# Kernel tuning notes

Hardware: AMD Instinct MI355X
Metric: run time of the kernel (lower is better)

Reference implementation:

```python
import jax, jax.numpy as jnp
import numpy as np
from jax import lax

B, N_ENT, D_ENT = 64, 512, 256
C_SCAT, C_MAP, W = 32, 18, 64
N_RES = 4


def conv2d(x, w, stride, pad):
    return lax.conv_general_dilated(x, w, (stride, stride), [(pad, pad), (pad, pad)],
                                    dimension_numbers=('NCHW', 'OIHW', 'NCHW'))


def batchnorm(x, g, b, eps=1e-5):
    # training-mode BN (batch statistics), matching nn.BatchNorm2d default train()
    mu = x.mean((0, 2, 3), keepdims=True)
    var = x.var((0, 2, 3), keepdims=True)
    return g[None, :, None, None] * (x - mu) * lax.rsqrt(var + eps) + b[None, :, None, None]


def setup_inputs() -> dict:
    key = jax.random.key(0)
    ks = jax.random.split(key, 24)
    s = 0.05
    inp = {
        'x': jax.random.uniform(ks[0], (B, C_MAP, W, W), jnp.float32),
        'entity_embeddings': jax.random.normal(ks[1], (B, N_ENT, D_ENT), jnp.float32),
        'entity_x_y': jax.random.randint(ks[2], (B, N_ENT, 16), 0, 2, jnp.int32),
        'conv1_w': jax.random.normal(ks[3], (C_SCAT, D_ENT), jnp.float32) * s,
        'project_w': jax.random.normal(ks[4], (32, C_SCAT + C_MAP, 1, 1), jnp.float32) * s,
        'project_b': jnp.zeros((32,), jnp.float32),
        'ds1_w': jax.random.normal(ks[5], (64, 32, 4, 4), jnp.float32) * s,
        'ds1_b': jnp.zeros((64,), jnp.float32),
        'ds2_w': jax.random.normal(ks[6], (128, 64, 4, 4), jnp.float32) * s,
        'ds2_b': jnp.zeros((128,), jnp.float32),
        'ds3_w': jax.random.normal(ks[7], (128, 128, 4, 4), jnp.float32) * s,
        'ds3_b': jnp.zeros((128,), jnp.float32),
        'res_conv1_w': jax.random.normal(ks[8], (N_RES, 128, 128, 3, 3), jnp.float32) * s,
        'res_bn1_g': jnp.ones((N_RES, 128), jnp.float32),
        'res_bn1_b': jnp.zeros((N_RES, 128), jnp.float32),
        'res_conv2_w': jax.random.normal(ks[9], (N_RES, 128, 128, 3, 3), jnp.float32) * s,
        'res_bn2_g': jnp.ones((N_RES, 128), jnp.float32),
        'res_bn2_b': jnp.zeros((N_RES, 128), jnp.float32),
        'fc_w': jax.random.normal(ks[10], (256, 8 * 8 * 128), jnp.float32) * s,
        'fc_b': jnp.zeros((256,), jnp.float32),
    }
    return inp


def _scatter(entity_embeddings, entity_x_y, conv1_w):
    # reduced = relu(Conv1d(256->32, k=1)) on entity dim
    reduced = jax.nn.relu(jnp.einsum('bnd,cd->bnc', entity_embeddings, conv1_w))  # [B,N,32]
    bits = entity_x_y
    pow2 = (2 ** jnp.arange(7, -1, -1)).astype(jnp.int32)
    xv = (bits[..., :8] * pow2).sum(-1) // 4   # [B,N] in 0..63
    yv = (bits[..., 8:] * pow2).sum(-1) // 4
    valid = (bits[..., 0] != -1000000000)
    reduced = reduced * valid[..., None].astype(reduced.dtype)
    b_idx = jnp.arange(entity_embeddings.shape[0], dtype=jnp.int32)[:, None]
    flat = (b_idx * (W * W) + yv * W + xv).reshape(-1)
    scat = jax.ops.segment_sum(reduced.reshape(-1, C_SCAT), flat, num_segments=entity_embeddings.shape[0] * W * W)
    return scat.reshape(-1, W, W, C_SCAT).transpose(0, 3, 1, 2)  # [B,32,W,W]


def reference(x, entity_embeddings, entity_x_y, conv1_w, project_w, project_b,
              ds1_w, ds1_b, ds2_w, ds2_b, ds3_w, ds3_b,
              res_conv1_w, res_bn1_g, res_bn1_b, res_conv2_w, res_bn2_g, res_bn2_b,
              fc_w, fc_b):
    scatter_map = _scatter(entity_embeddings, entity_x_y, conv1_w)
    h = jnp.concatenate([scatter_map, x], axis=1)  # [B,50,64,64]
    h = jax.nn.relu(conv2d(h, project_w, 1, 0) + project_b[None, :, None, None])
    h = jax.nn.relu(conv2d(h, ds1_w, 2, 1) + ds1_b[None, :, None, None])   # [B,64,32,32]
    h = jax.nn.relu(conv2d(h, ds2_w, 2, 1) + ds2_b[None, :, None, None])   # [B,128,16,16]
    h = jax.nn.relu(conv2d(h, ds3_w, 2, 1) + ds3_b[None, :, None, None])   # [B,128,8,8]
    map_skip = h
    for i in range(N_RES):
        identity = h
        o = batchnorm(conv2d(h, res_conv1_w[i], 1, 1), res_bn1_g[i], res_bn1_b[i])
        o = jax.nn.relu(o)
        o = batchnorm(conv2d(o, res_conv2_w[i], 1, 1), res_bn2_g[i], res_bn2_b[i])
        h = jax.nn.relu(o + identity)
        map_skip = map_skip + h
    flat = h.reshape(h.shape[0], -1)
    embedded_spatial = jax.nn.relu(flat @ fc_w.T + fc_b)
    return (map_skip, embedded_spatial)
```

## Files before the change

kernel.cpp:

```cpp
#include <hip/hip_runtime.h>
#include <hip/hip_bf16.h>

typedef __attribute__((ext_vector_type(8))) short bf16x8;
typedef __attribute__((ext_vector_type(4))) short bf16x4;
typedef __attribute__((ext_vector_type(4))) float f32x4;

__device__ __forceinline__ short f2bs(float v) {
  __hip_bfloat16 h = __float2bfloat16(v);
  return *reinterpret_cast<short*>(&h);
}

__global__ __launch_bounds__(256) void k_wall(
    const float* __restrict__ rc1w, const float* __restrict__ rc2w,
    const float* __restrict__ d1w, const float* __restrict__ d2w,
    const float* __restrict__ d3w, const float* __restrict__ fcw,
    const float* __restrict__ c1w, const float* __restrict__ pw,
    short* __restrict__ wTr1, short* __restrict__ wTr2, short* __restrict__ wTds1,
    short* __restrict__ wTds2, short* __restrict__ wTds3, short* __restrict__ wfcbf,
    short* __restrict__ wsc, short* __restrict__ wproj,
    float* __restrict__ scatz, float* __restrict__ statsz) {
  __shared__ float ld[128 * 65];
  const int bx = blockIdx.x;
  const int tid = threadIdx.x;
  if (bx < 512) {
    const float* src = (bx < 256) ? rc1w : rc2w;
    short* dst = (bx < 256) ? wTr1 : wTr2;
    const int cb = bx & 255;
    const float* sp = src + (size_t)cb * 2304;
#pragma unroll
    for (int r = 0; r < 9; ++r) ld[r * 256 + tid] = sp[r * 256 + tid];
    __syncthreads();
    const int g = cb * 256 + tid;
    const int layer = g >> 14, win = g & 16383;
    short* dp = dst + (size_t)layer * 147456 + win;
#pragma unroll
    for (int k = 0; k < 9; ++k) dp[k * 16384] = f2bs(ld[tid * 9 + k]);
  } else if (bx < 616) {
    int base, COCI;
    const float* src;
    short* dst;
    if (bx < 520) { base = 512; COCI = 2048; src = d1w; dst = wTds1; }
    else if (bx < 552) { base = 520; COCI = 8192; src = d2w; dst = wTds2; }
    else { base = 552; COCI = 16384; src = d3w; dst = wTds3; }
    const int cb = bx - base;
    const float* sp = src + (size_t)cb * 4096;
#pragma unroll
    for (int r = 0; r < 16; ++r) {
      const int j = r * 256 + tid;
      ld[j + (j >> 4)] = sp[j];
    }
    __syncthreads();
    const int g = cb * 256 + tid;
    short* dp = dst + g;
#pragma unroll
    for (int k = 0; k < 16; ++k) dp[(size_t)k * COCI] = f2bs(ld[tid * 17 + k]);
  } else if (bx < 872) {
    const int j = bx - 616;
    const float* sp = fcw + (size_t)j * 8192;
    for (int i = tid; i < 8192; i += 256) {
      const int co = i >> 6, pix = i & 63;
      ld[co * 65 + pix] = sp[i];
    }
    __syncthreads();
    short* dp = wfcbf + (size_t)j * 8192;
    for (int i = tid; i < 8192; i += 256) {
      const int pix = i >> 7, co = i & 127;
      dp[i] = f2bs(ld[co * 65 + pix]);
    }
  } else if (bx < 904) {
    const int i = (bx - 872) * 256 + tid;
    if (i < 8192) wsc[i] = f2bs(c1w[i]);
  } else if (bx < 912) {
    const int i = (bx - 904) * 256 + tid;
    if (i < 2048) {
      const int co = i >> 6, k = i & 63;
      wproj[i] = (k < 50) ? f2bs(pw[co * 50 + k]) : (short)0;
    }
  } else if (bx < 1424) {
    float4* dst = (float4*)(scatz + (size_t)(bx - 912) * 16384);
    const float4 z = {0.f, 0.f, 0.f, 0.f};
    for (int t = tid; t < 4096; t += 256) dst[t] = z;
  } else {
    for (int i = tid; i < 2064; i += 256) statsz[i] = 0.f;
  }
}

__global__ __launch_bounds__(256) void k_scatmfma(const float* __restrict__ emb,
                                                  const int* __restrict__ xy,
                                                  const short* __restrict__ wsc,
                                                  float* __restrict__ scat_pm) {
  constexpr int CIP = 264;
  __shared__ short abf[64 * CIP];
  __shared__ int flat[64];
  const int tid = threadIdx.x;
  const int e0 = blockIdx.x * 64;
  const float4* eg = (const float4*)(emb + (size_t)e0 * 256);
  for (int i = tid; i < 4096; i += 256) {
    const int e = i >> 6, k4 = i & 63;
    const float4 v = eg[(size_t)e * 64 + k4];
    bf16x4 o;
    o[0] = f2bs(v.x); o[1] = f2bs(v.y); o[2] = f2bs(v.z); o[3] = f2bs(v.w);
    *(bf16x4*)(&abf[e * CIP + k4 * 4]) = o;
  }
  if (tid < 64) {
    const int* bp = xy + (size_t)(e0 + tid) * 16;
    int xv = 0, yv = 0;
#pragma unroll
    for (int j = 0; j < 8; ++j) xv = (xv << 1) | bp[j];
#pragma unroll
    for (int j = 8; j < 16; ++j) yv = (yv << 1) | bp[j];
    flat[tid] = (bp[0] != -1000000000)
                    ? (((e0 + tid) >> 9) * 4096 + ((yv >> 2) << 6) + (xv >> 2))
                    : -1;
  }
  __syncthreads();
  const int wq = __builtin_amdgcn_readfirstlane(tid >> 6);
  const int lane = tid & 63;
  const int l15 = lane & 15, quad = lane >> 4;
  f32x4 acc[2];
  acc[0] = (f32x4){0.f, 0.f, 0.f, 0.f};
  acc[1] = (f32x4){0.f, 0.f, 0.f, 0.f};
  const short* arow = &abf[(wq * 16 + l15) * CIP + quad * 8];
  const short* w0 = wsc + (size_t)l15 * 256 + quad * 8;
  const short* w1 = wsc + (size_t)(16 + l15) * 256 + quad * 8;
#pragma unroll
  for (int kk = 0; kk < 8; ++kk) {
    bf16x8 a = *(const bf16x8*)(arow + kk * 32);
    acc[0] = __builtin_amdgcn_mfma_f32_16x16x32_bf16(a, *(const bf16x8*)(w0 + kk * 32), acc[0], 0, 0, 0);
    acc[1] = __builtin_amdgcn_mfma_f32_16x16x32_bf16(a, *(const bf16x8*)(w1 + kk * 32), acc[1], 0, 0, 0);
  }
#pragma unroll
  for (int nt = 0; nt < 2; ++nt)
#pragma unroll
    for (int r = 0; r < 4; ++r) {
      const int e = wq * 16 + quad * 4 + r;
      const float v = acc[nt][r];
      const int f = flat[e];
      if (f >= 0 && v > 0.f)
        atomicAdd(&scat_pm[(size_t)f * 32 + nt * 16 + l15], v);
    }
}

__global__ __launch_bounds__(256) void k_projmfma(const float* __restrict__ scat_pm,
                                                  const float* __restrict__ xin,
                                                  const short* __restrict__ wproj,
                                                  const float* __restrict__ pb,
                                                  short* __restrict__ h0pm) {
  constexpr int PK = 72;
  __shared__ short abf[128 * PK];
  const int tid = threadIdx.x;
  const int b = blockIdx.x >> 5;
  const int yx0 = (blockIdx.x & 31) << 7;
  const float4* sg = (const float4*)(scat_pm + ((size_t)(b * 4096 + yx0)) * 32);
  for (int i = tid; i < 1024; i += 256) {
    const int p = i >> 3, c4 = i & 7;
    const float4 v = sg[(size_t)p * 8 + c4];
    bf16x4 o;
    o[0] = f2bs(v.x); o[1] = f2bs(v.y); o[2] = f2bs(v.z); o[3] = f2bs(v.w);
    *(bf16x4*)(&abf[p * PK + c4 * 4]) = o;
  }
  for (int i = tid; i < 2304; i += 256) {
    const int run = i >> 7, p = i & 127;
    abf[p * PK + 32 + run] = f2bs(xin[(size_t)(b * 18 + run) * 4096 + yx0 + p]);
  }
  for (int i = tid; i < 2048; i += 256) {
    const int p = i >> 4, k = 50 + (i & 15);
    abf[p * PK + k] = 0;
  }
  __syncthreads();
  const int wq = __builtin_amdgcn_readfirstlane(tid >> 6);
  const int lane = tid & 63;
  const int l15 = lane & 15, quad = lane >> 4;
  f32x4 acc[2][2];
#pragma unroll
  for (int t = 0; t < 2; ++t)
#pragma unroll
    for (int n = 0; n < 2; ++n) acc[t][n] = (f32x4){0.f, 0.f, 0.f, 0.f};
  const short* wb0 = wproj + (size_t)l15 * 64 + quad * 8;
  const short* wb1 = wproj + (size_t)(16 + l15) * 64 + quad * 8;
#pragma unroll
  for (int kk = 0; kk < 2; ++kk) {
    const bf16x8 b0 = *(const bf16x8*)(wb0 + kk * 32);
    const bf16x8 b1 = *(const bf16x8*)(wb1 + kk * 32);
#pragma unroll
    for (int t = 0; t < 2; ++t) {
      const int pix = (wq * 2 + t) * 16 + l15;
      bf16x8 a = *(const bf16x8*)(&abf[pix * PK + quad * 8 + kk * 32]);
      acc[t][0] = __builtin_amdgcn_mfma_f32_16x16x32_bf16(a, b0, acc[t][0], 0, 0, 0);
      acc[t][1] = __builtin_amdgcn_mfma_f32_16x16x32_bf16(a, b1, acc[t][1], 0, 0, 0);
    }
  }
#pragma unroll
  for (int t = 0; t < 2; ++t)
#pragma unroll
    for (int n = 0; n < 2; ++n) {
      const int co = n * 16 + l15;
      const float bv = pb[co];
#pragma unroll
      for (int r = 0; r < 4; ++r) {
        const int pix = (wq * 2 + t) * 16 + quad * 4 + r;
        float v = acc[t][n][r] + bv;
        v = v > 0.f ? v : 0.f;
        h0pm[((size_t)(b * 4096 + yx0 + pix)) * 32 + co] = f2bs(v);
      }
    }
}

template <int CIN, int COUT, int HIN, int ROWSO, int COSPLIT, int MT, int NT, int OUTMODE>
__global__ __launch_bounds__(256) void k_ds2(const short* __restrict__ inpm,
                                             const short* __restrict__ wT,
                                             const float* __restrict__ bias,
                                             short* __restrict__ outbf,
                                             float* __restrict__ outf,
                                             float* __restrict__ msf) {
  constexpr int HOUT = HIN / 2;
  constexpr int ROWS = 2 * ROWSO + 2;
  constexpr int COLS = HIN + 2;
  constexpr int CHUNKS = CIN / 8;
  constexpr int KK = CIN / 32;
  constexpr int CIPAD = CIN + 8;
  constexpr int NHO = HOUT / ROWSO;
  __shared__ short lin[ROWS * COLS * CIPAD];
  const int tid = threadIdx.x;
  int bx = blockIdx.x;
  const int co_blk = (COSPLIT > 1) ? (bx % COSPLIT) : 0;
  if (COSPLIT > 1) bx /= COSPLIT;
  const int hoblk = bx % NHO;
  const int b = bx / NHO;
  for (int i = tid; i < ROWS * COLS * CHUNKS; i += 256) {
    const int ch = i % CHUNKS;
    const int pixv = i / CHUNKS;
    const int r = pixv / COLS, c = pixv % COLS;
    const int hi = 2 * ROWSO * hoblk - 1 + r;
    const int wc = c - 1;
    bf16x8 v = (bf16x8)(short)0;
    if (hi >= 0 && hi < HIN && wc >= 0 && wc < HIN)
      v = *(const bf16x8*)(inpm + ((size_t)(b * HIN + hi) * HIN + wc) * CIN + ch * 8);
    *(bf16x8*)(&lin[(r * COLS + c) * CIPAD + ch * 8]) = v;
  }
  __syncthreads();
  const int wq = __builtin_amdgcn_readfirstlane(tid >> 6);
  const int lane = tid & 63;
  const int l15 = lane & 15, quad = lane >> 4;
  const int mtile = (MT > 1) ? (wq % MT) : 0;
  const int cogrp = wq / MT;
  const int cobase = co_blk * (COUT / COSPLIT) + cogrp * (NT * 16);
  const int p = mtile * 16 + l15;
  const int dr = p / HOUT;
  const int col = p % HOUT;
  f32x4 acc[NT];
#pragma unroll
  for (int n = 0; n < NT; ++n) acc[n] = (f32x4){0.f, 0.f, 0.f, 0.f};
  const short* wrow = wT + (size_t)(cobase + l15) * CIN + quad * 8;
  for (int ky = 0; ky < 4; ++ky) {
    for (int kx = 0; kx < 4; ++kx) {
      const short* arow = &lin[((2 * dr + ky) * COLS + 2 * col + kx) * CIPAD + quad * 8];
      const short* wt = wrow + (size_t)(ky * 4 + kx) * COUT * CIN;
#pragma unroll
      for (int kk = 0; kk < KK; ++kk) {
        bf16x8 a = *(const bf16x8*)(arow + kk * 32);
#pragma unroll
        for (int n = 0; n < NT; ++n) {
          bf16x8 bf = *(const bf16x8*)(wt + n * 16 * CIN + kk * 32);
          acc[n] = __builtin_amdgcn_mfma_f32_16x16x32_bf16(a, bf, acc[n], 0, 0, 0);
        }
      }
    }
  }
#pragma unroll
  for (int n = 0; n < NT; ++n) {
    const int co = cobase + n * 16 + l15;
    const float bv = bias[co];
#pragma unroll
    for (int r = 0; r < 4; ++r) {
      const int pp = mtile * 16 + quad * 4 + r;
      const int dr2 = pp / HOUT;
      const int c2 = pp % HOUT;
      const int ho = hoblk * ROWSO + dr2;
      float v = acc[n][r] + bv;
      v = v > 0.f ? v : 0.f;
      const size_t o = ((size_t)b * HOUT * HOUT + ho * HOUT + c2) * COUT + co;
      outbf[o] = f2bs(v);
      if (OUTMODE == 1) {
        outf[o] = v;
        msf[o] = v;
      }
    }
  }
}

template <int BNIN>
__global__ __launch_bounds__(256) void k_resmfma(const short* __restrict__ hbfin,
                                                 const float* __restrict__ fin,
                                                 const float* __restrict__ statsIn,
                                                 const float* __restrict__ gIn,
                                                 const float* __restrict__ bIn,
                                                 const short* __restrict__ wT,
                                                 float* __restrict__ outpm,
                                                 float* __restrict__ statsOut) {
  constexpr int CIPAD = 136;
  __shared__ short lin[100 * CIPAD];
  __shared__ float bnsc[128], bnsh[128];
  const int tid = threadIdx.x;
  const int b = blockIdx.x >> 3;
  const int cobase = (blockIdx.x & 7) << 4;
  if (BNIN == 1) {
    if (tid < 128) {
      const float mu = statsIn[tid] * (1.f / 4096.f);
      const float var = statsIn[128 + tid] * (1.f / 4096.f) - mu * mu;
      const float sc = gIn[tid] * rsqrtf(var + 1e-5f);
      bnsc[tid] = sc;
      bnsh[tid] = bIn[tid] - mu * sc;
    }
    __syncthreads();
  }
  if (BNIN == 0) {
    const short* hb = hbfin + ((size_t)b << 13);
    for (int i = tid; i < 1600; i += 256) {
      const int pixel = i >> 4, ch = i & 15;
      const int r = pixel / 10, c = pixel % 10;
      bf16x8 v = (bf16x8)(short)0;
      if (r >= 1 && r <= 8 && c >= 1 && c <= 8)
        v = *(const bf16x8*)(hb + (((r - 1) << 3) + (c - 1)) * 128 + ch * 8);
      *(bf16x8*)(&lin[pixel * CIPAD + ch * 8]) = v;
    }
  } else {
    const float* fb = fin + ((size_t)b << 13);
    for (int i = tid; i < 3200; i += 256) {
      const int pixel = i >> 5, c4 = i & 31;
      const int r = pixel / 10, c = pixel % 10;
      bf16x4 o = (bf16x4)(short)0;
      if (r >= 1 && r <= 8 && c >= 1 && c <= 8) {
        const float4 x = *(const float4*)(fb + (size_t)(((r - 1) << 3) + (c - 1)) * 128 + c4 * 4);
        const float xv[4] = {x.x, x.y, x.z, x.w};
#pragma unroll
        for (int k = 0; k < 4; ++k) {
          const int ci = c4 * 4 + k;
          const float v = xv[k] * bnsc[ci] + bnsh[ci];
          o[k] = f2bs(v > 0.f ? v : 0.f);
        }
      }
      *(bf16x4*)(&lin[pixel * CIPAD + c4 * 4]) = o;
    }
  }
  __syncthreads();
  const int wq = __builtin_amdgcn_readfirstlane(tid >> 6);
  const int lane = tid & 63;
  const int l15 = lane & 15, quad = lane >> 4;
  const int p = wq * 16 + l15;
  const int py = p >> 3, px = p & 7;
  f32x4 acc = (f32x4){0.f, 0.f, 0.f, 0.f};
  const short* wrow = wT + (size_t)(cobase + l15) * 128 + quad * 8;
  for (int t = 0; t < 9; ++t) {
    const int ky = t / 3, kx = t % 3;
    const short* arow = &lin[((py + ky) * 10 + px + kx) * CIPAD + quad * 8];
    const short* wt = wrow + (size_t)t * 16384;
#pragma unroll
    for (int kk = 0; kk < 4; ++kk) {
      bf16x8 a = *(const bf16x8*)(arow + kk * 32);
      bf16x8 bf = *(const bf16x8*)(wt + kk * 32);
      acc = __builtin_amdgcn_mfma_f32_16x16x32_bf16(a, bf, acc, 0, 0, 0);
    }
  }
  float* ob = outpm + ((size_t)b << 13);
  const int co = cobase + l15;
  float s = 0.f, q = 0.f;
#pragma unroll
  for (int r = 0; r < 4; ++r) {
    const float v = acc[r];
    ob[(size_t)(wq * 16 + quad * 4 + r) * 128 + co] = v;
    s += v;
    q += v * v;
  }
  s += __shfl_down(s, 32); q += __shfl_down(q, 32);
  s += __shfl_down(s, 16); q += __shfl_down(q, 16);
  if (lane < 16) {
    atomicAdd(&statsOut[co], s);
    atomicAdd(&statsOut[128 + co], q);
  }
}

__global__ __launch_bounds__(256) void k_resA(const float* __restrict__ tmp2,
                                              const float* __restrict__ statsB,
                                              const float* __restrict__ g2,
                                              const float* __restrict__ b2,
                                              const float* __restrict__ identf,
                                              float* __restrict__ houtf,
                                              float* __restrict__ mspm,
                                              const short* __restrict__ wT,
                                              float* __restrict__ outpm,
                                              float* __restrict__ statsOut) {
  constexpr int CIPAD = 136;
  __shared__ short lin[100 * CIPAD];
  __shared__ float bnsc[128], bnsh[128];
  const int tid = threadIdx.x;
  const int b = blockIdx.x >> 3;
  const int cobase = (blockIdx.x & 7) << 4;
  if (tid < 128) {
    const float mu = statsB[tid] * (1.f / 4096.f);
    const float var = statsB[128 + tid] * (1.f / 4096.f) - mu * mu;
    const float sc = g2[tid] * rsqrtf(var + 1e-5f);
    bnsc[tid] = sc;
    bnsh[tid] = b2[tid] - mu * sc;
  }
  __syncthreads();
  const float* fb = tmp2 + ((size_t)b << 13);
  const float* idb = identf + ((size_t)b << 13);
  for (int t = tid; t < 3200; t += 256) {
    const int pixel = t >> 5, c4 = t & 31;
    const int r = pixel / 10, c = pixel % 10;
    bf16x4 o = (bf16x4)(short)0;
    if (r >= 1 && r <= 8 && c >= 1 && c <= 8) {
      const size_t p8 = (size_t)(((r - 1) << 3) + (c - 1)) * 128 + c4 * 4;
      const float4 x = *(const float4*)(fb + p8);
      const float4 id = *(const float4*)(idb + p8);
      const float xv[4] = {x.x, x.y, x.z, x.w};
      const float iv[4] = {id.x, id.y, id.z, id.w};
#pragma unroll
      for (int k = 0; k < 4; ++k) {
        const int ci = c4 * 4 + k;
        const float v = xv[k] * bnsc[ci] + bnsh[ci] + iv[k];
        o[k] = f2bs(v > 0.f ? v : 0.f);
      }
    }
    *(bf16x4*)(&lin[pixel * CIPAD + c4 * 4]) = o;
  }
  for (int t = tid; t < 1024; t += 256) {
    const int pix = t >> 4, cl = t & 15;
    const int cow = cobase + cl;
    const size_t o = ((size_t)b << 13) + (size_t)pix * 128 + cow;
    float v = tmp2[o] * bnsc[cow] + bnsh[cow] + identf[o];
    v = v > 0.f ? v : 0.f;
    houtf[o] = v;
    mspm[o] += v;
  }
  __syncthreads();
  const int wq = __builtin_amdgcn_readfirstlane(tid >> 6);
  const int lane = tid & 63;
  const int l15 = lane & 15, quad = lane >> 4;
  const int p = wq * 16 + l15;
  const int py = p >> 3, px = p & 7;
  f32x4 acc = (f32x4){0.f, 0.f, 0.f, 0.f};
  const short* wrow = wT + (size_t)(cobase + l15) * 128 + quad * 8;
  for (int t = 0; t < 9; ++t) {
    const int ky = t / 3, kx = t % 3;
    const short* arow = &lin[((py + ky) * 10 + px + kx) * CIPAD + quad * 8];
    const short* wt = wrow + (size_t)t * 16384;
#pragma unroll
    for (int kk = 0; kk < 4; ++kk) {
      bf16x8 a = *(const bf16x8*)(arow + kk * 32);
      bf16x8 bf = *(const bf16x8*)(wt + kk * 32);
      acc = __builtin_amdgcn_mfma_f32_16x16x32_bf16(a, bf, acc, 0, 0, 0);
    }
  }
  float* ob = outpm + ((size_t)b << 13);
  const int co = cobase + l15;
  float s = 0.f, q = 0.f;
#pragma unroll
  for (int r = 0; r < 4; ++r) {
    const float v = acc[r];
    ob[(size_t)(wq * 16 + quad * 4 + r) * 128 + co] = v;
    s += v;
    q += v * v;
  }
  s += __shfl_down(s, 32); q += __shfl_down(q, 32);
  s += __shfl_down(s, 16); q += __shfl_down(q, 16);
  if (lane < 16) {
    atomicAdd(&statsOut[co], s);
    atomicAdd(&statsOut[128 + co], q);
  }
}

__global__ __launch_bounds__(256) void k_msfin(const float* __restrict__ tmp2,
                                               const float* __restrict__ statsB,
                                               const float* __restrict__ g2,
                                               const float* __restrict__ b2,
                                               const float* __restrict__ identf,
                                               const float* __restrict__ mspm,
                                               short* __restrict__ hbf,
                                               float* __restrict__ out0) {
  __shared__ float t[64 * 133];
  __shared__ float bnsc[128], bnsh[128];
  const int b = blockIdx.x;
  const int tid = threadIdx.x;
  if (tid < 128) {
    const float mu = statsB[tid] * (1.f / 4096.f);
    const float var = statsB[128 + tid] * (1.f / 4096.f) - mu * mu;
    const float sc = g2[tid] * rsqrtf(var + 1e-5f);
    bnsc[tid] = sc;
    bnsh[tid] = b2[tid] - mu * sc;
  }
  __syncthreads();
  const size_t base = (size_t)b << 13;
  for (int i = tid; i < 8192; i += 256) {
    const int pix = i >> 7, co = i & 127;
    float v = tmp2[base + i] * bnsc[co] + bnsh[co] + identf[base + i];
    v = v > 0.f ? v : 0.f;
    hbf[base + i] = f2bs(v);
    t[pix * 133 + co] = mspm[base + i] + v;
  }
  __syncthreads();
  for (int i = tid; i < 8192; i += 256) {
    const int co = i >> 6, pix = i & 63;
    out0[base + i] = t[pix * 133 + co];
  }
}

__global__ __launch_bounds__(256) void k_fcmfma(const short* __restrict__ hbf,
                                                const short* __restrict__ wbf,
                                                float* __restrict__ part) {
  const int nb = blockIdx.x & 3;
  const int kb = blockIdx.x >> 2;
  const int wq = __builtin_amdgcn_readfirstlane((int)(threadIdx.x >> 6));
  const int lane = threadIdx.x & 63;
  const int l15 = lane & 15, quad = lane >> 4;
  const int k0 = kb * 256 + quad * 8;
  const short* wp = wbf + (size_t)(nb * 64 + wq * 16 + l15) * 8192 + k0;
  const short* hp = hbf + (size_t)l15 * 8192 + k0;
  f32x4 acc[4];
#pragma unroll
  for (int m = 0; m < 4; ++m) acc[m] = (f32x4){0.f, 0.f, 0.f, 0.f};
  for (int ks = 0; ks < 8; ++ks) {
    bf16x8 bfr = *(const bf16x8*)(wp + ks * 32);
#pragma unroll
    for (int m = 0; m < 4; ++m) {
      bf16x8 a = *(const bf16x8*)(hp + (size_t)m * 16 * 8192 + ks * 32);
      acc[m] = __builtin_amdgcn_mfma_f32_16x16x32_bf16(a, bfr, acc[m], 0, 0, 0);
    }
  }
#pragma unroll
  for (int m = 0; m < 4; ++m)
#pragma unroll
    for (int r = 0; r < 4; ++r) {
      const int b = m * 16 + quad * 4 + r;
      part[((size_t)kb * 64 + b) * 256 + nb * 64 + wq * 16 + l15] = acc[m][r];
    }
}

__global__ __launch_bounds__(256) void k_fcred(const float* __restrict__ part,
                                               const float* __restrict__ bias,
                                               float* __restrict__ out1) {
  const int idx = blockIdx.x * 256 + threadIdx.x;
  const int j = idx & 255;
  float s = 0.f;
#pragma unroll 8
  for (int kb = 0; kb < 32; ++kb) s += part[(size_t)kb * 16384 + idx];
  const float v = s + bias[j];
  out1[idx] = v > 0.f ? v : 0.f;
}

extern "C" void kernel_launch(void* const* d_in, const int* in_sizes, int n_in,
                              void* d_out, int out_size, void* d_ws, size_t ws_size,
                              hipStream_t stream) {
  const float* xin = (const float*)d_in[0];
  const float* emb = (const float*)d_in[1];
  const int* xy = (const int*)d_in[2];
  const float* c1w = (const float*)d_in[3];
  const float* pw = (const float*)d_in[4];
  const float* pb = (const float*)d_in[5];
  const float* d1w = (const float*)d_in[6];
  const float* d1b = (const float*)d_in[7];
  const float* d2w = (const float*)d_in[8];
  const float* d2b = (const float*)d_in[9];
  const float* d3w = (const float*)d_in[10];
  const float* d3b = (const float*)d_in[11];
  const float* rc1w = (const float*)d_in[12];
  const float* rbn1g = (const float*)d_in[13];
  const float* rbn1b = (const float*)d_in[14];
  const float* rc2w = (const float*)d_in[15];
  const float* rbn2g = (const float*)d_in[16];
  const float* rbn2b = (const float*)d_in[17];
  const float* fcw = (const float*)d_in[18];
  const float* fcb = (const float*)d_in[19];

  float* out0 = (float*)d_out;
  float* out1 = out0 + 524288;

  float* F = (float*)d_ws;
  float* scat = F + 0;
  short* h1pm = (short*)(F + 0);
  short* h2pm = (short*)(F + 2097152);
  float* hApm = F + 3145728;
  float* hBpm = F + 3670016;
  float* tmppm = F + 4194304;
  float* tmp2pm = F + 4718592;
  float* mspm = F + 5242880;
  short* pmbfA = (short*)(F + 5767168);
  short* hbf = (short*)(F + 6029312);
  float* stats = F + 6291456;
  float* fcpart = F + 6293504;
  short* h0pm = (short*)(F + 8388608);
  short* wfcbf = (short*)(F + 12582912);
  short* wTr1 = (short*)(F + 13631488);
  short* wTr2 = wTr1 + 589824;
  short* wTds1 = wTr2 + 589824;
  short* wTds2 = wTds1 + 32768;
  short* wTds3 = wTds2 + 131072;
  short* wsc = wTds3 + 262144;
  short* wproj = wsc + 8192;

  k_wall<<<1425, 256, 0, stream>>>(rc1w, rc2w, d1w, d2w, d3w, fcw, c1w, pw,
                                   wTr1, wTr2, wTds1, wTds2, wTds3, wfcbf, wsc, wproj,
                                   scat, stats);
  k_scatmfma<<<512, 256, 0, stream>>>(emb, xy, wsc, scat);
  k_projmfma<<<2048, 256, 0, stream>>>(scat, xin, wproj, pb, h0pm);
  k_ds2<32, 64, 64, 2, 1, 4, 4, 0><<<1024, 256, 0, stream>>>(h0pm, wTds1, d1b, h1pm, nullptr, nullptr);
  k_ds2<64, 128, 32, 1, 1, 1, 2, 0><<<1024, 256, 0, stream>>>(h1pm, wTds2, d2b, h2pm, nullptr, nullptr);
  k_ds2<128, 128, 16, 2, 2, 1, 1, 1><<<512, 256, 0, stream>>>(h2pm, wTds3, d3b, pmbfA, hApm, mspm);

  k_resmfma<0><<<512, 256, 0, stream>>>(pmbfA, nullptr, nullptr, nullptr, nullptr,
                                        wTr1, tmppm, stats);
  k_resmfma<1><<<512, 256, 0, stream>>>(nullptr, tmppm, stats, rbn1g, rbn1b,
                                        wTr2, tmp2pm, stats + 256);
  float* idp = hApm;
  float* hop = hBpm;
  for (int i = 1; i < 4; ++i) {
    k_resA<<<512, 256, 0, stream>>>(tmp2pm, stats + (i - 1) * 512 + 256,
                                    rbn2g + (i - 1) * 128, rbn2b + (i - 1) * 128,
                                    idp, hop, mspm, wTr1 + (size_t)i * 147456,
                                    tmppm, stats + i * 512);
    k_resmfma<1><<<512, 256, 0, stream>>>(nullptr, tmppm, stats + i * 512,
                                          rbn1g + i * 128, rbn1b + i * 128,
                                          wTr2 + (size_t)i * 147456, tmp2pm,
                                          stats + i * 512 + 256);
    float* sw = idp; idp = hop; hop = sw;
  }
  k_msfin<<<64, 256, 0, stream>>>(tmp2pm, stats + 3 * 512 + 256, rbn2g + 3 * 128,
                                  rbn2b + 3 * 128, idp, mspm, hbf, out0);
  k_fcmfma<<<128, 256, 0, stream>>>(hbf, wfcbf, fcpart);
  k_fcred<<<64, 256, 0, stream>>>(fcpart, fcb, out1);
}
```

Baseline: 401.8 us.

## Fuse residual tower into one persistent kernel with grid-wide BN barriers

Replaces the nine per-stage residual-block launches (resmfma/resA/msfin) with a single 64-block, 512-thread kernel. Each block owns one image and keeps the identity and map_skip values in registers. Batch-norm statistics are shared across the grid through atomics and a spin-wait counter barrier. This removes launch overhead and the fp32 intermediate round trips through global memory. In exchange it uses only 64 workgroups, and correctness depends on all blocks being co-resident and on the counter being reset each call. The counter sits next to the fcpart buffer, so if it is not cleared every call the barrier may not hold.

```diff
diff --git a/kernel.cpp b/kernel.cpp
--- a/kernel.cpp
+++ b/kernel.cpp
@@ -211,8 +211,7 @@
                                              const short* __restrict__ wT,
                                              const float* __restrict__ bias,
                                              short* __restrict__ outbf,
-                                             float* __restrict__ outf,
-                                             float* __restrict__ msf) {
+                                             float* __restrict__ outf) {
   constexpr int HOUT = HIN / 2;
   constexpr int ROWS = 2 * ROWSO + 2;
   constexpr int COLS = HIN + 2;
@@ -280,229 +279,173 @@
       float v = acc[n][r] + bv;
       v = v > 0.f ? v : 0.f;
       const size_t o = ((size_t)b * HOUT * HOUT + ho * HOUT + c2) * COUT + co;
-      outbf[o] = f2bs(v);
-      if (OUTMODE == 1) {
-        outf[o] = v;
-        msf[o] = v;
-      }
-    }
-  }
-}
-
-template <int BNIN>
-__global__ __launch_bounds__(256) void k_resmfma(const short* __restrict__ hbfin,
-                                                 const float* __restrict__ fin,
-                                                 const float* __restrict__ statsIn,
-                                                 const float* __restrict__ gIn,
-                                                 const float* __restrict__ bIn,
-                                                 const short* __restrict__ wT,
-                                                 float* __restrict__ outpm,
-                                                 float* __restrict__ statsOut) {
+      if constexpr (OUTMODE != 2) outbf[o] = f2bs(v);
+      else outf[o] = v;
+    }
+  }
+}
+
+__device__ __forceinline__ void statsync(unsigned* cnt, unsigned target) {
+  __syncthreads();
+  if (threadIdx.x == 0) {
+    __hip_atomic_fetch_add(cnt, 1u, __ATOMIC_RELAXED, __HIP_MEMORY_SCOPE_AGENT);
+    while (__hip_atomic_load(cnt, __ATOMIC_RELAXED, __HIP_MEMORY_SCOPE_AGENT) < target)
+      __builtin_amdgcn_s_sleep(1);
+  }
+  __syncthreads();
+}
+
+__global__ __launch_bounds__(512) void k_res4(
+    const float* __restrict__ hf32,
+    const short* __restrict__ wTr1, const short* __restrict__ wTr2,
+    const float* __restrict__ rbn1g, const float* __restrict__ rbn1b,
+    const float* __restrict__ rbn2g, const float* __restrict__ rbn2b,
+    float* __restrict__ stats, unsigned* __restrict__ cnt,
+    short* __restrict__ hbf, float* __restrict__ out0) {
   constexpr int CIPAD = 136;
   __shared__ short lin[100 * CIPAD];
-  __shared__ float bnsc[128], bnsh[128];
   const int tid = threadIdx.x;
-  const int b = blockIdx.x >> 3;
-  const int cobase = (blockIdx.x & 7) << 4;
-  if (BNIN == 1) {
-    if (tid < 128) {
-      const float mu = statsIn[tid] * (1.f / 4096.f);
-      const float var = statsIn[128 + tid] * (1.f / 4096.f) - mu * mu;
-      const float sc = gIn[tid] * rsqrtf(var + 1e-5f);
-      bnsc[tid] = sc;
-      bnsh[tid] = bIn[tid] - mu * sc;
-    }
+  const int b = blockIdx.x;
+  const int w = __builtin_amdgcn_readfirstlane(tid >> 6);
+  const int lane = tid & 63;
+  const int l15 = lane & 15, quad = lane >> 4;
+  const int co = w * 16 + l15;
+  for (int i = tid; i < 1700; i += 512) *(bf16x8*)(&lin[i * 8]) = (bf16x8)(short)0;
+  float hloc[16], msloc[16];
+  {
+    const float* hf = hf32 + ((size_t)b << 13);
+#pragma unroll
+    for (int j = 0; j < 16; ++j) {
+      const int pix = (j >> 2) * 16 + quad * 4 + (j & 3);
+      const float v = hf[(size_t)pix * 128 + co];
+      hloc[j] = v;
+      msloc[j] = v;
+    }
+  }
+  unsigned ph = 0;
+  for (int i = 0; i < 4; ++i) {
+    float* sA = stats + i * 512;
+    float* sB = sA + 256;
     __syncthreads();
-  }
-  if (BNIN == 0) {
-    const short* hb = hbfin + ((size_t)b << 13);
-    for (int i = tid; i < 1600; i += 256) {
-      const int pixel = i >> 4, ch = i & 15;
-      const int r = pixel / 10, c = pixel % 10;
-      bf16x8 v = (bf16x8)(short)0;
-      if (r >= 1 && r <= 8 && c >= 1 && c <= 8)
-        v = *(const bf16x8*)(hb + (((r - 1) << 3) + (c - 1)) * 128 + ch * 8);
-      *(bf16x8*)(&lin[pixel * CIPAD + ch * 8]) = v;
-    }
-  } else {
-    const float* fb = fin + ((size_t)b << 13);
-    for (int i = tid; i < 3200; i += 256) {
-      const int pixel = i >> 5, c4 = i & 31;
-      const int r = pixel / 10, c = pixel % 10;
-      bf16x4 o = (bf16x4)(short)0;
-      if (r >= 1 && r <= 8 && c >= 1 && c <= 8) {
-        const float4 x = *(const float4*)(fb + (size_t)(((r - 1) << 3) + (c - 1)) * 128 + c4 * 4);
-        const float xv[4] = {x.x, x.y, x.z, x.w};
-#pragma unroll
-        for (int k = 0; k < 4; ++k) {
-          const int ci = c4 * 4 + k;
-          const float v = xv[k] * bnsc[ci] + bnsh[ci];
-          o[k] = f2bs(v > 0.f ? v : 0.f);
+#pragma unroll
+    for (int j = 0; j < 16; ++j) {
+      const int pix = (j >> 2) * 16 + quad * 4 + (j & 3);
+      const int py = pix >> 3, px = pix & 7;
+      lin[((py + 1) * 10 + px + 1) * CIPAD + co] = f2bs(hloc[j]);
+    }
+    __syncthreads();
+    f32x4 acc[4];
+#pragma unroll
+    for (int m = 0; m < 4; ++m) acc[m] = (f32x4){0.f, 0.f, 0.f, 0.f};
+    {
+      const short* wrow = wTr1 + (size_t)i * 147456 + (size_t)co * 128 + quad * 8;
+      for (int t = 0; t < 9; ++t) {
+        const int ky = t / 3, kx = t % 3;
+        const short* wt = wrow + (size_t)t * 16384;
+#pragma unroll
+        for (int kk = 0; kk < 4; ++kk) {
+          const bf16x8 bfr = *(const bf16x8*)(wt + kk * 32);
+#pragma unroll
+          for (int m = 0; m < 4; ++m) {
+            const int pA = m * 16 + l15;
+            const int py = pA >> 3, px = pA & 7;
+            const bf16x8 a =
+                *(const bf16x8*)(&lin[((py + ky) * 10 + px + kx) * CIPAD + quad * 8 + kk * 32]);
+            acc[m] = __builtin_amdgcn_mfma_f32_16x16x32_bf16(a, bfr, acc[m], 0, 0, 0);
+          }
         }
       }
-      *(bf16x4*)(&lin[pixel * CIPAD + c4 * 4]) = o;
-    }
-  }
-  __syncthreads();
-  const int wq = __builtin_amdgcn_readfirstlane(tid >> 6);
-  const int lane = tid & 63;
-  const int l15 = lane & 15, quad = lane >> 4;
-  const int p = wq * 16 + l15;
-  const int py = p >> 3, px = p & 7;
-  f32x4 acc = (f32x4){0.f, 0.f, 0.f, 0.f};
-  const short* wrow = wT + (size_t)(cobase + l15) * 128 + quad * 8;
-  for (int t = 0; t < 9; ++t) {
-    const int ky = t / 3, kx = t % 3;
-    const short* arow = &lin[((py + ky) * 10 + px + kx) * CIPAD + quad * 8];
-    const short* wt = wrow + (size_t)t * 16384;
-#pragma unroll
-    for (int kk = 0; kk < 4; ++kk) {
-      bf16x8 a = *(const bf16x8*)(arow + kk * 32);
-      bf16x8 bf = *(const bf16x8*)(wt + kk * 32);
-      acc = __builtin_amdgcn_mfma_f32_16x16x32_bf16(a, bf, acc, 0, 0, 0);
-    }
-  }
-  float* ob = outpm + ((size_t)b << 13);
-  const int co = cobase + l15;
-  float s = 0.f, q = 0.f;
-#pragma unroll
-  for (int r = 0; r < 4; ++r) {
-    const float v = acc[r];
-    ob[(size_t)(wq * 16 + quad * 4 + r) * 128 + co] = v;
-    s += v;
-    q += v * v;
-  }
-  s += __shfl_down(s, 32); q += __shfl_down(q, 32);
-  s += __shfl_down(s, 16); q += __shfl_down(q, 16);
-  if (lane < 16) {
-    atomicAdd(&statsOut[co], s);
-    atomicAdd(&statsOut[128 + co], q);
-  }
-}
-
-__global__ __launch_bounds__(256) void k_resA(const float* __restrict__ tmp2,
-                                              const float* __restrict__ statsB,
-                                              const float* __restrict__ g2,
-                                              const float* __restrict__ b2,
-                                              const float* __restrict__ identf,
-                                              float* __restrict__ houtf,
-                                              float* __restrict__ mspm,
-                                              const short* __restrict__ wT,
-                                              float* __restrict__ outpm,
-                                              float* __restrict__ statsOut) {
-  constexpr int CIPAD = 136;
-  __shared__ short lin[100 * CIPAD];
-  __shared__ float bnsc[128], bnsh[128];
-  const int tid = threadIdx.x;
-  const int b = blockIdx.x >> 3;
-  const int cobase = (blockIdx.x & 7) << 4;
-  if (tid < 128) {
-    const float mu = statsB[tid] * (1.f / 4096.f);
-    const float var = statsB[128 + tid] * (1.f / 4096.f) - mu * mu;
-    const float sc = g2[tid] * rsqrtf(var + 1e-5f);
-    bnsc[tid] = sc;
-    bnsh[tid] = b2[tid] - mu * sc;
-  }
-  __syncthreads();
-  const float* fb = tmp2 + ((size_t)b << 13);
-  const float* idb = identf + ((size_t)b << 13);
-  for (int t = tid; t < 3200; t += 256) {
-    const int pixel = t >> 5, c4 = t & 31;
-    const int r = pixel / 10, c = pixel % 10;
-    bf16x4 o = (bf16x4)(short)0;
-    if (r >= 1 && r <= 8 && c >= 1 && c <= 8) {
-      const size_t p8 = (size_t)(((r - 1) << 3) + (c - 1)) * 128 + c4 * 4;
-      const float4 x = *(const float4*)(fb + p8);
-      const float4 id = *(const float4*)(idb + p8);
-      const float xv[4] = {x.x, x.y, x.z, x.w};
-      const float iv[4] = {id.x, id.y, id.z, id.w};
-#pragma unroll
-      for (int k = 0; k < 4; ++k) {
-        const int ci = c4 * 4 + k;
-        const float v = xv[k] * bnsc[ci] + bnsh[ci] + iv[k];
-        o[k] = f2bs(v > 0.f ? v : 0.f);
+    }
+    {
+      float s = 0.f, q = 0.f;
+#pragma unroll
+      for (int m = 0; m < 4; ++m)
+#pragma unroll
+        for (int r = 0; r < 4; ++r) { const float v = acc[m][r]; s += v; q += v * v; }
+      s += __shfl_down(s, 32); q += __shfl_down(q, 32);
+      s += __shfl_down(s, 16); q += __shfl_down(q, 16);
+      if (lane < 16) {
+        atomicAdd(&sA[w * 16 + lane], s);
+        atomicAdd(&sA[128 + w * 16 + lane], q);
       }
     }
-    *(bf16x4*)(&lin[pixel * CIPAD + c4 * 4]) = o;
-  }
-  for (int t = tid; t < 1024; t += 256) {
-    const int pix = t >> 4, cl = t & 15;
-    const int cow = cobase + cl;
-    const size_t o = ((size_t)b << 13) + (size_t)pix * 128 + cow;
-    float v = tmp2[o] * bnsc[cow] + bnsh[cow] + identf[o];
-    v = v > 0.f ? v : 0.f;
-    houtf[o] = v;
-    mspm[o] += v;
-  }
-  __syncthreads();
-  const int wq = __builtin_amdgcn_readfirstlane(tid >> 6);
-  const int lane = tid & 63;
-  const int l15 = lane & 15, quad = lane >> 4;
-  const int p = wq * 16 + l15;
-  const int py = p >> 3, px = p & 7;
-  f32x4 acc = (f32x4){0.f, 0.f, 0.f, 0.f};
-  const short* wrow = wT + (size_t)(cobase + l15) * 128 + quad * 8;
-  for (int t = 0; t < 9; ++t) {
-    const int ky = t / 3, kx = t % 3;
-    const short* arow = &lin[((py + ky) * 10 + px + kx) * CIPAD + quad * 8];
-    const short* wt = wrow + (size_t)t * 16384;
-#pragma unroll
-    for (int kk = 0; kk < 4; ++kk) {
-      bf16x8 a = *(const bf16x8*)(arow + kk * 32);
-      bf16x8 bf = *(const bf16x8*)(wt + kk * 32);
-      acc = __builtin_amdgcn_mfma_f32_16x16x32_bf16(a, bf, acc, 0, 0, 0);
-    }
-  }
-  float* ob = outpm + ((size_t)b << 13);
-  const int co = cobase + l15;
-  float s = 0.f, q = 0.f;
-#pragma unroll
-  for (int r = 0; r < 4; ++r) {
-    const float v = acc[r];
-    ob[(size_t)(wq * 16 + quad * 4 + r) * 128 + co] = v;
-    s += v;
-    q += v * v;
-  }
-  s += __shfl_down(s, 32); q += __shfl_down(q, 32);
-  s += __shfl_down(s, 16); q += __shfl_down(q, 16);
-  if (lane < 16) {
-    atomicAdd(&statsOut[co], s);
-    atomicAdd(&statsOut[128 + co], q);
-  }
-}
-
-__global__ __launch_bounds__(256) void k_msfin(const float* __restrict__ tmp2,
-                                               const float* __restrict__ statsB,
-                                               const float* __restrict__ g2,
-                                               const float* __restrict__ b2,
-                                               const float* __restrict__ identf,
-                                               const float* __restrict__ mspm,
-                                               short* __restrict__ hbf,
-                                               float* __restrict__ out0) {
-  __shared__ float t[64 * 133];
-  __shared__ float bnsc[128], bnsh[128];
-  const int b = blockIdx.x;
-  const int tid = threadIdx.x;
-  if (tid < 128) {
-    const float mu = statsB[tid] * (1.f / 4096.f);
-    const float var = statsB[128 + tid] * (1.f / 4096.f) - mu * mu;
-    const float sc = g2[tid] * rsqrtf(var + 1e-5f);
-    bnsc[tid] = sc;
-    bnsh[tid] = b2[tid] - mu * sc;
-  }
-  __syncthreads();
-  const size_t base = (size_t)b << 13;
-  for (int i = tid; i < 8192; i += 256) {
-    const int pix = i >> 7, co = i & 127;
-    float v = tmp2[base + i] * bnsc[co] + bnsh[co] + identf[base + i];
-    v = v > 0.f ? v : 0.f;
-    hbf[base + i] = f2bs(v);
-    t[pix * 133 + co] = mspm[base + i] + v;
-  }
-  __syncthreads();
-  for (int i = tid; i < 8192; i += 256) {
-    const int co = i >> 6, pix = i & 63;
-    out0[base + i] = t[pix * 133 + co];
+    statsync(cnt, 64u * (++ph));
+    {
+      const float mu = __hip_atomic_load(&sA[co], __ATOMIC_RELAXED, __HIP_MEMORY_SCOPE_AGENT) * (1.f / 4096.f);
+      const float ex2 = __hip_atomic_load(&sA[128 + co], __ATOMIC_RELAXED, __HIP_MEMORY_SCOPE_AGENT) * (1.f / 4096.f);
+      const float sc1 = rbn1g[i * 128 + co] * rsqrtf(ex2 - mu * mu + 1e-5f);
+      const float sh1 = rbn1b[i * 128 + co] - mu * sc1;
+#pragma unroll
+      for (int m = 0; m < 4; ++m)
+#pragma unroll
+        for (int r = 0; r < 4; ++r) {
+          const int pix = m * 16 + quad * 4 + r;
+          const int py = pix >> 3, px = pix & 7;
+          const float v = acc[m][r] * sc1 + sh1;
+          lin[((py + 1) * 10 + px + 1) * CIPAD + co] = f2bs(v > 0.f ? v : 0.f);
+        }
+    }
+    __syncthreads();
+#pragma unroll
+    for (int m = 0; m < 4; ++m) acc[m] = (f32x4){0.f, 0.f, 0.f, 0.f};
+    {
+      const short* wrow = wTr2 + (size_t)i * 147456 + (size_t)co * 128 + quad * 8;
+      for (int t = 0; t < 9; ++t) {
+        const int ky = t / 3, kx = t % 3;
+        const short* wt = wrow + (size_t)t * 16384;
+#pragma unroll
+        for (int kk = 0; kk < 4; ++kk) {
+          const bf16x8 bfr = *(const bf16x8*)(wt + kk * 32);
+#pragma unroll
+          for (int m = 0; m < 4; ++m) {
+            const int pA = m * 16 + l15;
+            const int py = pA >> 3, px = pA & 7;
+            const bf16x8 a =
+                *(const bf16x8*)(&lin[((py + ky) * 10 + px + kx) * CIPAD + quad * 8 + kk * 32]);
+            acc[m] = __builtin_amdgcn_mfma_f32_16x16x32_bf16(a, bfr, acc[m], 0, 0, 0);
+          }
+        }
+      }
+    }
+    {
+      float s = 0.f, q = 0.f;
+#pragma unroll
+      for (int m = 0; m < 4; ++m)
+#pragma unroll
+        for (int r = 0; r < 4; ++r) { const float v = acc[m][r]; s += v; q += v * v; }
+      s += __shfl_down(s, 32); q += __shfl_down(q, 32);
+      s += __shfl_down(s, 16); q += __shfl_down(q, 16);
+      if (lane < 16) {
+        atomicAdd(&sB[w * 16 + lane], s);
+        atomicAdd(&sB[128 + w * 16 + lane], q);
+      }
+    }
+    statsync(cnt, 64u * (++ph));
+    {
+      const float mu = __hip_atomic_load(&sB[co], __ATOMIC_RELAXED, __HIP_MEMORY_SCOPE_AGENT) * (1.f / 4096.f);
+      const float ex2 = __hip_atomic_load(&sB[128 + co], __ATOMIC_RELAXED, __HIP_MEMORY_SCOPE_AGENT) * (1.f / 4096.f);
+      const float sc2 = rbn2g[i * 128 + co] * rsqrtf(ex2 - mu * mu + 1e-5f);
+      const float sh2 = rbn2b[i * 128 + co] - mu * sc2;
+#pragma unroll
+      for (int m = 0; m < 4; ++m)
+#pragma unroll
+        for (int r = 0; r < 4; ++r) {
+          float v = acc[m][r] * sc2 + sh2 + hloc[m * 4 + r];
+          v = v > 0.f ? v : 0.f;
+          hloc[m * 4 + r] = v;
+          msloc[m * 4 + r] += v;
+        }
+    }
+  }
+  {
+    float* ob = out0 + ((size_t)b << 13) + (size_t)co * 64;
+    short* hb = hbf + ((size_t)b << 13);
+#pragma unroll
+    for (int j = 0; j < 16; ++j) {
+      const int pix = (j >> 2) * 16 + quad * 4 + (j & 3);
+      ob[pix] = msloc[j];
+      hb[(size_t)pix * 128 + co] = f2bs(hloc[j]);
+    }
   }
 }
 
@@ -580,14 +523,10 @@
   float* scat = F + 0;
   short* h1pm = (short*)(F + 0);
   short* h2pm = (short*)(F + 2097152);
-  float* hApm = F + 3145728;
-  float* hBpm = F + 3670016;
-  float* tmppm = F + 4194304;
-  float* tmp2pm = F + 4718592;
-  float* mspm = F + 5242880;
-  short* pmbfA = (short*)(F + 5767168);
-  short* hbf = (short*)(F + 6029312);
+  float* hf32 = F + 3145728;
+  short* hbf = (short*)(F + 5242880);
   float* stats = F + 6291456;
+  unsigned* cnt = (unsigned*)(stats + 2048);
   float* fcpart = F + 6293504;
   short* h0pm = (short*)(F + 8388608);
   short* wfcbf = (short*)(F + 12582912);
@@ -604,29 +543,11 @@
                                    scat, stats);
   k_scatmfma<<<512, 256, 0, stream>>>(emb, xy, wsc, scat);
   k_projmfma<<<2048, 256, 0, stream>>>(scat, xin, wproj, pb, h0pm);
-  k_ds2<32, 64, 64, 2, 1, 4, 4, 0><<<1024, 256, 0, stream>>>(h0pm, wTds1, d1b, h1pm, nullptr, nullptr);
-  k_ds2<64, 128, 32, 1, 1, 1, 2, 0><<<1024, 256, 0, stream>>>(h1pm, wTds2, d2b, h2pm, nullptr, nullptr);
-  k_ds2<128, 128, 16, 2, 2, 1, 1, 1><<<512, 256, 0, stream>>>(h2pm, wTds3, d3b, pmbfA, hApm, mspm);
-
-  k_resmfma<0><<<512, 256, 0, stream>>>(pmbfA, nullptr, nullptr, nullptr, nullptr,
-                                        wTr1, tmppm, stats);
-  k_resmfma<1><<<512, 256, 0, stream>>>(nullptr, tmppm, stats, rbn1g, rbn1b,
-                                        wTr2, tmp2pm, stats + 256);
-  float* idp = hApm;
-  float* hop = hBpm;
-  for (int i = 1; i < 4; ++i) {
-    k_resA<<<512, 256, 0, stream>>>(tmp2pm, stats + (i - 1) * 512 + 256,
-                                    rbn2g + (i - 1) * 128, rbn2b + (i - 1) * 128,
-                                    idp, hop, mspm, wTr1 + (size_t)i * 147456,
-                                    tmppm, stats + i * 512);
-    k_resmfma<1><<<512, 256, 0, stream>>>(nullptr, tmppm, stats + i * 512,
-                                          rbn1g + i * 128, rbn1b + i * 128,
-                                          wTr2 + (size_t)i * 147456, tmp2pm,
-                                          stats + i * 512 + 256);
-    float* sw = idp; idp = hop; hop = sw;
-  }
-  k_msfin<<<64, 256, 0, stream>>>(tmp2pm, stats + 3 * 512 + 256, rbn2g + 3 * 128,
-                                  rbn2b + 3 * 128, idp, mspm, hbf, out0);
+  k_ds2<32, 64, 64, 2, 1, 4, 4, 0><<<1024, 256, 0, stream>>>(h0pm, wTds1, d1b, h1pm, nullptr);
+  k_ds2<64, 128, 32, 1, 1, 1, 2, 0><<<1024, 256, 0, stream>>>(h1pm, wTds2, d2b, h2pm, nullptr);
+  k_ds2<128, 128, 16, 2, 2, 1, 1, 2><<<512, 256, 0, stream>>>(h2pm, wTds3, d3b, nullptr, hf32);
+  k_res4<<<64, 512, 0, stream>>>(hf32, wTr1, wTr2, rbn1g, rbn1b, rbn2g, rbn2b,
+                                 stats, cnt, hbf, out0);
   k_fcmfma<<<128, 256, 0, stream>>>(hbf, wfcbf, fcpart);
   k_fcred<<<64, 256, 0, stream>>>(fcpart, fcb, out1);
 }
```

After: 343.3 us. -14.6%, faster.
